# Optimization experiments

Measured on AMD Instinct MI355X. Metric: run time of the kernel, lower is better.

## Reference

```python
import jax, jax.numpy as jnp
import numpy as np

B, N, K = 128, 512, 6      # graphs, nodes per graph, kNN neighbors
IN_FEAT, POS_DIM, H = 128, 3, 256
NB = B * N                  # total nodes
EPS_BN = 1e-5


def setup_inputs() -> dict:
    key = jax.random.key(0)
    ks = jax.random.split(key, 32)
    inp = {
        "x": jax.random.normal(ks[0], (NB, IN_FEAT), dtype=jnp.float32),
        "pos": jax.random.normal(ks[1], (NB, POS_DIM), dtype=jnp.float32) * 5.0,
    }
    d_in = IN_FEAT + POS_DIM
    def lin(k, fi, fo):
        s = 1.0 / np.sqrt(fi)
        return jax.random.uniform(k, (fi, fo), jnp.float32, -s, s)
    # GCN layers
    inp["W1"] = lin(ks[2], d_in, H); inp["b1"] = jnp.zeros((H,), jnp.float32)
    inp["W2"] = lin(ks[3], H, H);    inp["b2"] = jnp.zeros((H,), jnp.float32)
    inp["W3"] = lin(ks[4], H, H);    inp["b3"] = jnp.zeros((H,), jnp.float32)
    # BatchNorm (eval mode: running stats)
    for i, km, kv in [(1, ks[5], ks[6]), (2, ks[7], ks[8]), (3, ks[9], ks[10])]:
        inp[f"g{i}"]  = jnp.ones((H,), jnp.float32)
        inp[f"be{i}"] = jnp.zeros((H,), jnp.float32)
        inp[f"m{i}"]  = jax.random.normal(km, (H,), jnp.float32) * 0.1
        inp[f"v{i}"]  = jax.random.uniform(kv, (H,), jnp.float32, 0.5, 1.5)
    # attention gate, heads
    inp["gate_w"] = lin(ks[11], H, 1); inp["gate_b"] = jnp.zeros((1,), jnp.float32)
    inp["aff_w"]  = lin(ks[12], H, 1); inp["aff_b"]  = jnp.zeros((1,), jnp.float32)
    inp["rl_w1"]  = lin(ks[13], H, H); inp["rl_b1"]  = jnp.zeros((H,), jnp.float32)
    inp["rl_w2"]  = lin(ks[14], H, POS_DIM); inp["rl_b2"] = jnp.zeros((POS_DIM,), jnp.float32)
    return inp


def _knn_edges(pos):
    # torch_geometric knn_graph semantics: per-graph k nearest neighbors,
    # no self loops, edges (neighbor -> node).  batch = repeat(arange(B), N).
    p = pos.reshape(B, N, POS_DIM)
    sq = jnp.sum(p * p, axis=-1)                                  # [B,N]
    d2 = sq[:, :, None] + sq[:, None, :] - 2.0 * jnp.einsum("bnd,bmd->bnm", p, p)
    d2 = jnp.where(jnp.eye(N, dtype=bool)[None], jnp.inf, d2)     # exclude self
    _, idx = jax.lax.top_k(-d2, K)                                # [B,N,K] local nbr ids
    offs = (jnp.arange(B) * N)[:, None, None]
    src = (idx + offs).reshape(-1)                                # neighbor (source)
    dst = jnp.repeat(jnp.arange(NB), K)                           # target node
    return src, dst


def _gcn(h, W, b, src, dst):
    # GCNConv: add self loops, symmetric norm D^-1/2 (A+I) D^-1/2
    hw = h @ W                                                    # [NB,H]
    deg = jax.ops.segment_sum(jnp.ones_like(dst, jnp.float32), dst, num_segments=NB) + 1.0
    dis = jax.lax.rsqrt(deg)
    norm = dis[src] * dis[dst]                                    # [E]
    agg = jax.ops.segment_sum(hw[src] * norm[:, None], dst, num_segments=NB)
    agg = agg + hw * (1.0 / deg)[:, None]                          # self loop term
    return agg + b


def _bn(h, g, be, m, v):
    return (h - m) * (g * jax.lax.rsqrt(v + EPS_BN)) + be


def reference(x, pos, W1, b1, W2, b2, W3, b3,
              g1, be1, m1, v1, g2, be2, m2, v2, g3, be3, m3, v3,
              gate_w, gate_b, aff_w, aff_b, rl_w1, rl_b1, rl_w2, rl_b2):
    src, dst = _knn_edges(pos)
    h = jnp.concatenate([x, pos], axis=1)                          # [NB, in_feat+3]
    h = jax.nn.relu(_bn(_gcn(h, W1, b1, src, dst), g1, be1, m1, v1))
    h = jax.nn.relu(_bn(_gcn(h, W2, b2, src, dst), g2, be2, m2, v2))
    h = jax.nn.relu(_bn(_gcn(h, W3, b3, src, dst), g3, be3, m3, v3))
    # (dropout is identity in eval mode)
    gate = jax.nn.relu(h @ gate_w + gate_b)[:, 0]                  # [NB]
    attn = jax.nn.softmax(gate.reshape(B, N), axis=1)              # scatter_softmax over batch
    gemb = jnp.einsum("bn,bnh->bh", attn, h.reshape(B, N, H))      # scatter_add of weighted x
    affinity = gemb @ aff_w + aff_b                                # [B,1]
    pose = jax.nn.relu(gemb @ rl_w1 + rl_b1) @ rl_w2 + rl_b2        # [B,3]
    return affinity, pose
```

## Files before the change

### kernel.cpp

```cpp
#include <hip/hip_runtime.h>
#include <hip/hip_bf16.h>
#include <math.h>
#include <float.h>

#define NBG 128
#define NND 512
#define KNN 6
#define NB_TOT (NBG*NND)
#define HF 256
#define NSTEP1 5

typedef short bf16x8 __attribute__((ext_vector_type(8)));
typedef float f32x4 __attribute__((ext_vector_type(4)));

__device__ __forceinline__ int swzoff(int row, int kbyte) {
    return (row*64 + kbyte) ^ (((row>>1)&3)<<4);
}

__device__ __forceinline__ void split_store(const float* v, char* hi_p, char* lo_p) {
    bf16x8 hi, lo;
    #pragma unroll
    for (int j = 0; j < 8; ++j) {
        __hip_bfloat16 h = __float2bfloat16(v[j]);
        float hf = __bfloat162float(h);
        __hip_bfloat16 l = __float2bfloat16(v[j] - hf);
        hi[j] = *(short*)&h;
        lo[j] = *(short*)&l;
    }
    *(bf16x8*)hi_p = hi;
    *(bf16x8*)lo_p = lo;
}

__device__ __forceinline__ int xcd_swz(int bid, int grid) {
    return (bid & 7) * (grid >> 3) + (bid >> 3);
}

__global__ __launch_bounds__(256) void knn_kernel(const float* __restrict__ pos,
                                                  unsigned short* __restrict__ nbr)
{
    const int blk = blockIdx.x;
    const int g = blk >> 3;
    const int chunk = (blk & 7) * 64;
    const int tid = threadIdx.x;
    const int node = chunk + (tid >> 2);
    const int sub = tid & 3;

    __shared__ float4 p4[NND + (NND>>6)];
    const float* pg = pos + (size_t)g * NND * 3;
    for (int n = tid; n < NND; n += 256) {
        float x = pg[n*3+0], y = pg[n*3+1], z = pg[n*3+2];
        p4[n + (n>>6)] = make_float4(x, y, z, x*x + y*y + z*z);
    }
    __syncthreads();

    const float4 pi = p4[node + (node>>6)];
    const float m2x = -2.0f*pi.x, m2y = -2.0f*pi.y, m2z = -2.0f*pi.z;

    float bdA[KNN], bdB[KNN]; int biA[KNN], biB[KNN];
    #pragma unroll
    for (int q = 0; q < KNN; ++q) {
        bdA[q] = FLT_MAX; biA[q] = 0x7fffffff;
        bdB[q] = FLT_MAX; biB[q] = 0x7fffffff;
    }

    const int j0 = sub * 128;
    const float4* baseA = &p4[sub*130];
    const float4* baseB = &p4[sub*130 + 65];

    #pragma unroll 2
    for (int t = 0; t < 64; ++t) {
        int ja = j0 + t, jb = j0 + 64 + t;
        float4 pa = baseA[t];
        float4 pb = baseB[t];
        float da = fmaf(m2z, pa.z, fmaf(m2y, pa.y, fmaf(m2x, pa.x, pa.w)));
        float db = fmaf(m2z, pb.z, fmaf(m2y, pb.y, fmaf(m2x, pb.x, pb.w)));
        da = (ja == node) ? FLT_MAX : da;
        db = (jb == node) ? FLT_MAX : db;
        float ca = da; int ia = ja;
        float cb = db; int ib = jb;
        #pragma unroll
        for (int q = 0; q < KNN; ++q) {
            bool sa = ca < bdA[q];
            float t1 = sa ? ca : bdA[q]; float t2 = sa ? bdA[q] : ca;
            int   t3 = sa ? ia : biA[q]; int   t4 = sa ? biA[q] : ia;
            bdA[q] = t1; ca = t2; biA[q] = t3; ia = t4;
            bool sb = cb < bdB[q];
            float u1 = sb ? cb : bdB[q]; float u2 = sb ? bdB[q] : cb;
            int   u3 = sb ? ib : biB[q]; int   u4 = sb ? biB[q] : ib;
            bdB[q] = u1; cb = u2; biB[q] = u3; ib = u4;
        }
    }

    float ld[KNN]; int li[KNN];
    #pragma unroll
    for (int q = 0; q < KNN; ++q) {
        float ad = bdA[q], xd = bdB[KNN-1-q];
        int   ai = biA[q], xi = biB[KNN-1-q];
        bool t = (ad < xd) || (ad == xd && ai < xi);
        ld[q] = t ? ad : xd;
        li[q] = t ? ai : xi;
    }
    #pragma unroll
    for (int pass = 0; pass < KNN-1; ++pass)
        #pragma unroll
        for (int a = 0; a < KNN-1-pass; ++a) {
            int b = a+1;
            bool sw = (ld[b] < ld[a]) || (ld[b] == ld[a] && li[b] < li[a]);
            float td = sw ? ld[b] : ld[a]; float ud = sw ? ld[a] : ld[b];
            int   ti = sw ? li[b] : li[a]; int   ui = sw ? li[a] : li[b];
            ld[a] = td; li[a] = ti; ld[b] = ud; li[b] = ui;
        }

    #pragma unroll
    for (int mi = 0; mi < 2; ++mi) {
        const int mask = 1 << mi;
        float od[KNN]; int oi[KNN];
        #pragma unroll
        for (int q = 0; q < KNN; ++q) {
            od[q] = __shfl_xor(ld[q], mask);
            oi[q] = __shfl_xor(li[q], mask);
        }
        #pragma unroll
        for (int q = 0; q < KNN; ++q) {
            float ad = ld[q], xd = od[KNN-1-q];
            int   ai = li[q], xi = oi[KNN-1-q];
            bool t = (ad < xd) || (ad == xd && ai < xi);
            ld[q] = t ? ad : xd;
            li[q] = t ? ai : xi;
        }
        #pragma unroll
        for (int pass = 0; pass < KNN-1; ++pass)
            #pragma unroll
            for (int a = 0; a < KNN-1-pass; ++a) {
                int b = a+1;
                bool sw = (ld[b] < ld[a]) || (ld[b] == ld[a] && li[b] < li[a]);
                float td = sw ? ld[b] : ld[a]; float ud = sw ? ld[a] : ld[b];
                int   ti = sw ? li[b] : li[a]; int   ui = sw ? li[a] : li[b];
                ld[a] = td; li[a] = ti; ld[b] = ud; li[b] = ui;
            }
    }

    if (sub == 0) {
        int base = (g*NND + node)*KNN;
        #pragma unroll
        for (int q = 0; q < KNN; ++q) nbr[base+q] = (unsigned short)li[q];
    }
}

__global__ __launch_bounds__(256) void prew_all(
    const float* __restrict__ W1, const float* __restrict__ W2,
    const float* __restrict__ W3,
    char* __restrict__ I1, char* __restrict__ I2, char* __restrict__ I3)
{
    int b = blockIdx.x;
    const float* W; char* img; int K, nstep;
    if (b < 20)      { W = W1; img = I1; K = 131; nstep = 5; }
    else if (b < 52) { W = W2; img = I2; K = 256; nstep = 8; b -= 20; }
    else             { W = W3; img = I3; K = 256; nstep = 8; b -= 52; }
    int gid = b*256 + threadIdx.x;
    int per_nb = nstep*512;
    int nb = gid / per_nb;
    int r  = gid - nb*per_nb;
    int step = r >> 9;
    int r2 = r & 511;
    int cl = r2 >> 2;
    int kc = (r2 & 3) * 8;
    float v[8];
    #pragma unroll
    for (int j = 0; j < 8; ++j) {
        int gk = step*32 + kc + j;
        v[j] = (gk < K) ? W[(size_t)gk*256 + nb*128 + cl] : 0.f;
    }
    char* base = img + (size_t)nb*nstep*16384 + (size_t)step*16384;
    int off = swzoff(cl, kc*2);
    split_store(v, base + off, base + 8192 + off);
}

__global__ __launch_bounds__(256) void agg_first(const float* __restrict__ x,
                                                 const float* __restrict__ pos,
                                                 const unsigned short* __restrict__ nbr,
                                                 char* __restrict__ Aimg)
{
    int gid = xcd_swz(blockIdx.x, gridDim.x)*256 + threadIdx.x;
    int i = gid / 20, ch = gid - i*20;
    const float rs = 1.0f/sqrtf(7.0f);
    const float c1 = rs*rs, c2 = 1.0f/7.0f;
    const int gbase = i & ~(NND-1);
    float v[8];
    if (ch < 16) {
        int jn[KNN];
        #pragma unroll
        for (int q = 0; q < KNN; ++q) jn[q] = gbase + nbr[i*KNN+q];
        const float4* x4 = (const float4*)x;
        int c4 = ch*2;
        float4 s0 = x4[(size_t)i*32 + c4], s1 = x4[(size_t)i*32 + c4 + 1];
        float a0=0,a1=0,a2=0,a3=0,b0=0,b1=0,b2=0,b3=0;
        #pragma unroll
        for (int q = 0; q < KNN; ++q) {
            float4 t0 = x4[(size_t)jn[q]*32 + c4];
            float4 t1 = x4[(size_t)jn[q]*32 + c4 + 1];
            a0+=t0.x; a1+=t0.y; a2+=t0.z; a3+=t0.w;
            b0+=t1.x; b1+=t1.y; b2+=t1.z; b3+=t1.w;
        }
        v[0]=a0*c1+s0.x*c2; v[1]=a1*c1+s0.y*c2; v[2]=a2*c1+s0.z*c2; v[3]=a3*c1+s0.w*c2;
        v[4]=b0*c1+s1.x*c2; v[5]=b1*c1+s1.y*c2; v[6]=b2*c1+s1.z*c2; v[7]=b3*c1+s1.w*c2;
    } else if (ch == 16) {
        int jn[KNN];
        #pragma unroll
        for (int q = 0; q < KNN; ++q) jn[q] = gbase + nbr[i*KNN+q];
        float ax=0, ay=0, az=0;
        #pragma unroll
        for (int q = 0; q < KNN; ++q) {
            ax += pos[(size_t)jn[q]*3+0];
            ay += pos[(size_t)jn[q]*3+1];
            az += pos[(size_t)jn[q]*3+2];
        }
        v[0] = ax*c1 + pos[(size_t)i*3+0]*c2;
        v[1] = ay*c1 + pos[(size_t)i*3+1]*c2;
        v[2] = az*c1 + pos[(size_t)i*3+2]*c2;
        v[3]=v[4]=v[5]=v[6]=v[7]=0.f;
    } else {
        #pragma unroll
        for (int j = 0; j < 8; ++j) v[j] = 0.f;
    }
    int mb = i >> 7, row = i & 127, step = ch >> 2, kbyte = (ch & 3)*16;
    char* base = Aimg + (size_t)mb*(NSTEP1*16384) + (size_t)step*16384;
    int off = swzoff(row, kbyte);
    split_store(v, base + off, base + 8192 + off);
}

__global__ __launch_bounds__(256) void agg_h(const float* __restrict__ h,
                                             const unsigned short* __restrict__ nbr,
                                             char* __restrict__ Aimg)
{
    int gid = xcd_swz(blockIdx.x, gridDim.x)*256 + threadIdx.x;
    int i = gid >> 5, ch = gid & 31;
    const float rs = 1.0f/sqrtf(7.0f);
    const float c1 = rs*rs, c2 = 1.0f/7.0f;
    const int gbase = i & ~(NND-1);
    int jn[KNN];
    #pragma unroll
    for (int q = 0; q < KNN; ++q) jn[q] = gbase + nbr[i*KNN+q];
    const float4* h4 = (const float4*)h;
    int c4 = ch*2;
    float4 s0 = h4[(size_t)i*64 + c4], s1 = h4[(size_t)i*64 + c4 + 1];
    float a0=0,a1=0,a2=0,a3=0,b0=0,b1=0,b2=0,b3=0;
    #pragma unroll
    for (int q = 0; q < KNN; ++q) {
        float4 t0 = h4[(size_t)jn[q]*64 + c4];
        float4 t1 = h4[(size_t)jn[q]*64 + c4 + 1];
        a0+=t0.x; a1+=t0.y; a2+=t0.z; a3+=t0.w;
        b0+=t1.x; b1+=t1.y; b2+=t1.z; b3+=t1.w;
    }
    float v[8];
    v[0]=a0*c1+s0.x*c2; v[1]=a1*c1+s0.y*c2; v[2]=a2*c1+s0.z*c2; v[3]=a3*c1+s0.w*c2;
    v[4]=b0*c1+s1.x*c2; v[5]=b1*c1+s1.y*c2; v[6]=b2*c1+s1.z*c2; v[7]=b3*c1+s1.w*c2;
    int mb = i >> 7, row = i & 127, step = ch >> 2, kbyte = (ch & 3)*16;
    char* base = Aimg + (size_t)mb*(8*16384) + (size_t)step*16384;
    int off = swzoff(row, kbyte);
    split_store(v, base + off, base + 8192 + off);
}

__global__ __launch_bounds__(256,4) void gemm_mfma(
    const char* __restrict__ Aimg, const char* __restrict__ Wimg, int nstep,
    const float* __restrict__ bias,
    const float* __restrict__ gam, const float* __restrict__ bet,
    const float* __restrict__ mu,  const float* __restrict__ var,
    float* __restrict__ out)
{
    __shared__ uint4 lds4[34816/16];
    char* lds  = (char*)lds4;
    char* Alds = lds;
    char* Wlds = lds + 16384;
    float* scs = (float*)(lds + 32768);
    float* shs = scs + 256;
    const int tid = threadIdx.x;
    const int lane = tid & 63, wave = tid >> 6;
    const int wm = wave >> 1, wn = wave & 1;
    const int mblk = blockIdx.x, nblk = blockIdx.y;

    if (tid < 256) {
        float s = gam[tid] / sqrtf(var[tid] + 1e-5f);
        scs[tid] = s;
        shs[tid] = bet[tid] + (bias[tid] - mu[tid]) * s;
    }

    const char* Ab = Aimg + (size_t)mblk * nstep * 16384;
    const char* Wb = Wimg + (size_t)nblk * nstep * 16384;

    const char* gbase; char* lbase;
    int soff;
    if (wave < 2) { gbase = Ab;  lbase = Alds; soff = wave*8192; }
    else          { gbase = Wb;  lbase = Wlds; soff = (wave-2)*8192; }

    f32x4 acc[4][4];
    #pragma unroll
    for (int m = 0; m < 4; ++m)
        #pragma unroll
        for (int n = 0; n < 4; ++n) acc[m][n] = (f32x4){0.f,0.f,0.f,0.f};

    for (int s = 0; s < nstep; ++s) {
        #pragma unroll
        for (int i = 0; i < 8; ++i) {
            int off = soff + i*1024;
            __builtin_amdgcn_global_load_lds(
                (const __attribute__((address_space(1))) void*)(gbase + (size_t)s*16384 + off + lane*16),
                (__attribute__((address_space(3))) void*)(lbase + off), 16, 0, 0);
        }
        __syncthreads();
        const int kb = (lane >> 4) * 16;
        bf16x8 ah[4], al[4];
        #pragma unroll
        for (int m = 0; m < 4; ++m) {
            int row = wm*64 + m*16 + (lane & 15);
            int off = swzoff(row, kb);
            ah[m] = *(const bf16x8*)(Alds + off);
            al[m] = *(const bf16x8*)(Alds + 8192 + off);
        }
        #pragma unroll
        for (int n = 0; n < 4; ++n) {
            int col = wn*64 + n*16 + (lane & 15);
            int off = swzoff(col, kb);
            bf16x8 bh = *(const bf16x8*)(Wlds + off);
            bf16x8 bl = *(const bf16x8*)(Wlds + 8192 + off);
            #pragma unroll
            for (int m = 0; m < 4; ++m) {
                acc[m][n] = __builtin_amdgcn_mfma_f32_16x16x32_bf16(ah[m], bh, acc[m][n], 0, 0, 0);
                acc[m][n] = __builtin_amdgcn_mfma_f32_16x16x32_bf16(al[m], bh, acc[m][n], 0, 0, 0);
                acc[m][n] = __builtin_amdgcn_mfma_f32_16x16x32_bf16(ah[m], bl, acc[m][n], 0, 0, 0);
            }
        }
        __syncthreads();
    }

    #pragma unroll
    for (int n = 0; n < 4; ++n) {
        int c = nblk*128 + wn*64 + n*16 + (lane & 15);
        float sc = scs[c], sh = shs[c];
        #pragma unroll
        for (int m = 0; m < 4; ++m) {
            int r0 = mblk*128 + wm*64 + m*16 + (lane >> 4)*4;
            #pragma unroll
            for (int q = 0; q < 4; ++q) {
                float v = acc[m][n][q]*sc + sh;
                out[(size_t)(r0+q)*256 + c] = fmaxf(v, 0.f);
            }
        }
    }
}

__global__ __launch_bounds__(256) void gate_kernel(const float* __restrict__ h3,
                                                   const float* __restrict__ gate_w,
                                                   const float* __restrict__ gate_b,
                                                   float* __restrict__ gate)
{
    const int lane = threadIdx.x & 63;
    const int gw = (blockIdx.x*256 + threadIdx.x) >> 6;
    float4 w4 = ((const float4*)gate_w)[lane];
    float gb = gate_b[0];
    #pragma unroll
    for (int it = 0; it < 4; ++it) {
        int r = gw + it*8192;
        float4 v = ((const float4*)(h3 + (size_t)r*HF))[lane];
        float s = v.x*w4.x + v.y*w4.y + v.z*w4.z + v.w*w4.w;
        #pragma unroll
        for (int o = 32; o > 0; o >>= 1) s += __shfl_xor(s, o, 64);
        if (lane == 0) gate[r] = fmaxf(s + gb, 0.f);
    }
}

__device__ __forceinline__ float blk_sum256(float v, volatile float* red)
{
    #pragma unroll
    for (int o = 32; o > 0; o >>= 1) v += __shfl_xor(v, o, 64);
    __syncthreads();
    if ((threadIdx.x & 63) == 0) red[threadIdx.x >> 6] = v;
    __syncthreads();
    return (red[0] + red[1]) + (red[2] + red[3]);
}

__global__ __launch_bounds__(256) void gemb_kernel(const float* __restrict__ h3,
                                                   const float* __restrict__ gate,
                                                   float* __restrict__ gembp)
{
    const int g = blockIdx.x, s = blockIdx.y;
    const int tid = threadIdx.x, lane = tid & 63, w = tid >> 6;
    __shared__ float at[128];
    __shared__ float red4[4][HF];
    __shared__ float red[4];

    float g0 = gate[g*NND + tid];
    float g1 = gate[g*NND + 256 + tid];
    float m = fmaxf(g0, g1);
    #pragma unroll
    for (int o = 32; o > 0; o >>= 1) m = fmaxf(m, __shfl_xor(m, o, 64));
    if ((tid & 63) == 0) red[tid >> 6] = m;
    __syncthreads();
    m = fmaxf(fmaxf(red[0], red[1]), fmaxf(red[2], red[3]));
    float S = blk_sum256(expf(g0 - m) + expf(g1 - m), red);
    if (tid < 128) at[tid] = expf(gate[g*NND + s*128 + tid] - m) / S;
    __syncthreads();

    const float* hb = h3 + (size_t)(g*NND + s*128 + w*32) * HF;
    float4 acc = make_float4(0.f, 0.f, 0.f, 0.f);
    #pragma unroll 4
    for (int n = 0; n < 32; ++n) {
        float a = at[w*32 + n];
        float4 v = ((const float4*)(hb + (size_t)n*HF))[lane];
        acc.x = fmaf(a, v.x, acc.x); acc.y = fmaf(a, v.y, acc.y);
        acc.z = fmaf(a, v.z, acc.z); acc.w = fmaf(a, v.w, acc.w);
    }
    *(float4*)&red4[w][lane*4] = acc;
    __syncthreads();
    if (tid < HF) {
        float sum = (red4[0][tid] + red4[1][tid]) + (red4[2][tid] + red4[3][tid]);
        gembp[((size_t)s*NBG + g)*HF + tid] = sum;
    }
}

__global__ __launch_bounds__(256) void heads_kernel(
    const float* __restrict__ gembp,
    const float* __restrict__ aff_w,  const float* __restrict__ aff_b,
    const float* __restrict__ rl_w1,  const float* __restrict__ rl_b1,
    const float* __restrict__ rl_w2,  const float* __restrict__ rl_b2,
    float* __restrict__ out)
{
    int g = blockIdx.x, tid = threadIdx.x;
    __shared__ float gemb[HF];
    __shared__ float red[4];
    float acc = (gembp[((size_t)0*NBG + g)*HF + tid] + gembp[((size_t)1*NBG + g)*HF + tid])
              + (gembp[((size_t)2*NBG + g)*HF + tid] + gembp[((size_t)3*NBG + g)*HF + tid]);
    gemb[tid] = acc;
    __syncthreads();

    float sa = blk_sum256(acc * aff_w[tid], red);
    if (tid == 0) out[g] = sa + aff_b[0];

    float t = rl_b1[tid];
    #pragma unroll 4
    for (int k2 = 0; k2 < HF; ++k2)
        t = fmaf(gemb[k2], rl_w1[(size_t)k2*HF + tid], t);
    t = fmaxf(t, 0.f);
    float s0 = blk_sum256(t * rl_w2[(size_t)tid*3 + 0], red);
    if (tid == 0) out[128 + g*3 + 0] = s0 + rl_b2[0];
    float s1 = blk_sum256(t * rl_w2[(size_t)tid*3 + 1], red);
    if (tid == 0) out[128 + g*3 + 1] = s1 + rl_b2[1];
    float s2 = blk_sum256(t * rl_w2[(size_t)tid*3 + 2], red);
    if (tid == 0) out[128 + g*3 + 2] = s2 + rl_b2[2];
}

extern "C" void kernel_launch(void* const* d_in, const int* in_sizes, int n_in,
                              void* d_out, int out_size, void* d_ws, size_t ws_size,
                              hipStream_t stream)
{
    const float* x      = (const float*)d_in[0];
    const float* pos    = (const float*)d_in[1];
    const float* W1     = (const float*)d_in[2];
    const float* b1     = (const float*)d_in[3];
    const float* W2     = (const float*)d_in[4];
    const float* b2     = (const float*)d_in[5];
    const float* W3     = (const float*)d_in[6];
    const float* b3     = (const float*)d_in[7];
    const float* g1     = (const float*)d_in[8];
    const float* be1    = (const float*)d_in[9];
    const float* m1     = (const float*)d_in[10];
    const float* v1     = (const float*)d_in[11];
    const float* g2     = (const float*)d_in[12];
    const float* be2    = (const float*)d_in[13];
    const float* m2     = (const float*)d_in[14];
    const float* v2     = (const float*)d_in[15];
    const float* g3     = (const float*)d_in[16];
    const float* be3    = (const float*)d_in[17];
    const float* m3     = (const float*)d_in[18];
    const float* v3     = (const float*)d_in[19];
    const float* gate_w = (const float*)d_in[20];
    const float* gate_b = (const float*)d_in[21];
    const float* aff_w  = (const float*)d_in[22];
    const float* aff_b  = (const float*)d_in[23];
    const float* rl_w1  = (const float*)d_in[24];
    const float* rl_b1  = (const float*)d_in[25];
    const float* rl_w2  = (const float*)d_in[26];
    const float* rl_b2  = (const float*)d_in[27];
    float* out = (float*)d_out;

    char* wsb = (char*)d_ws;
    unsigned short* nbr = (unsigned short*)wsb;
    char* Wimg1 = wsb + 786432;
    char* Wimg2 = Wimg1 + (size_t)2*NSTEP1*16384;
    char* Wimg3 = Wimg2 + (size_t)2*8*16384;
    float* h    = (float*)(Wimg3 + (size_t)2*8*16384);
    char* Aimg  = (char*)(h + (size_t)NB_TOT*HF);
    float* gate  = (float*)Aimg;
    float* gembp = gate + NB_TOT;

    knn_kernel<<<NBG*8, 256, 0, stream>>>(pos, nbr);
    prew_all<<<84, 256, 0, stream>>>(W1, W2, W3, Wimg1, Wimg2, Wimg3);

    agg_first<<<(NB_TOT*20)/256, 256, 0, stream>>>(x, pos, nbr, Aimg);
    gemm_mfma<<<dim3(NB_TOT/128, 2), 256, 0, stream>>>(Aimg, Wimg1, NSTEP1,
        b1, g1, be1, m1, v1, h);
    agg_h<<<(NB_TOT*32)/256, 256, 0, stream>>>(h, nbr, Aimg);
    gemm_mfma<<<dim3(NB_TOT/128, 2), 256, 0, stream>>>(Aimg, Wimg2, 8,
        b2, g2, be2, m2, v2, h);
    agg_h<<<(NB_TOT*32)/256, 256, 0, stream>>>(h, nbr, Aimg);
    gemm_mfma<<<dim3(NB_TOT/128, 2), 256, 0, stream>>>(Aimg, Wimg3, 8,
        b3, g3, be3, m3, v3, h);

    gate_kernel<<<2048, 256, 0, stream>>>(h, gate_w, gate_b, gate);
    gemb_kernel<<<dim3(NBG, 4), 256, 0, stream>>>(h, gate, gembp);
    heads_kernel<<<NBG, 256, 0, stream>>>(gembp, aff_w, aff_b,
                                          rl_w1, rl_b1, rl_w2, rl_b2, out);
}
```

Measured before the change: 241.6 us.

## Fuse neighbor aggregation into GEMM for GCN layers 2 and 3

Replaces the separate agg_h kernel and the gemm_mfma launch for layers 2 and 3 with one gcn_fused kernel. Each 512-thread block gathers the neighbor-averaged features for its 128 rows straight into LDS as split bf16, then multiplies against the full 256-column weight. This removes the round trip of the split-bf16 A image through global memory and two kernel launches per layer. In exchange, the gather latency is no longer overlapped across separate kernels, occupancy drops to 2 blocks per CU, and ping-pong h buffers are needed.

```diff
diff --git a/kernel.cpp b/kernel.cpp
--- a/kernel.cpp
+++ b/kernel.cpp
@@ -229,38 +229,6 @@
     split_store(v, base + off, base + 8192 + off);
 }
 
-__global__ __launch_bounds__(256) void agg_h(const float* __restrict__ h,
-                                             const unsigned short* __restrict__ nbr,
-                                             char* __restrict__ Aimg)
-{
-    int gid = xcd_swz(blockIdx.x, gridDim.x)*256 + threadIdx.x;
-    int i = gid >> 5, ch = gid & 31;
-    const float rs = 1.0f/sqrtf(7.0f);
-    const float c1 = rs*rs, c2 = 1.0f/7.0f;
-    const int gbase = i & ~(NND-1);
-    int jn[KNN];
-    #pragma unroll
-    for (int q = 0; q < KNN; ++q) jn[q] = gbase + nbr[i*KNN+q];
-    const float4* h4 = (const float4*)h;
-    int c4 = ch*2;
-    float4 s0 = h4[(size_t)i*64 + c4], s1 = h4[(size_t)i*64 + c4 + 1];
-    float a0=0,a1=0,a2=0,a3=0,b0=0,b1=0,b2=0,b3=0;
-    #pragma unroll
-    for (int q = 0; q < KNN; ++q) {
-        float4 t0 = h4[(size_t)jn[q]*64 + c4];
-        float4 t1 = h4[(size_t)jn[q]*64 + c4 + 1];
-        a0+=t0.x; a1+=t0.y; a2+=t0.z; a3+=t0.w;
-        b0+=t1.x; b1+=t1.y; b2+=t1.z; b3+=t1.w;
-    }
-    float v[8];
-    v[0]=a0*c1+s0.x*c2; v[1]=a1*c1+s0.y*c2; v[2]=a2*c1+s0.z*c2; v[3]=a3*c1+s0.w*c2;
-    v[4]=b0*c1+s1.x*c2; v[5]=b1*c1+s1.y*c2; v[6]=b2*c1+s1.z*c2; v[7]=b3*c1+s1.w*c2;
-    int mb = i >> 7, row = i & 127, step = ch >> 2, kbyte = (ch & 3)*16;
-    char* base = Aimg + (size_t)mb*(8*16384) + (size_t)step*16384;
-    int off = swzoff(row, kbyte);
-    split_store(v, base + off, base + 8192 + off);
-}
-
 __global__ __launch_bounds__(256,4) void gemm_mfma(
     const char* __restrict__ Aimg, const char* __restrict__ Wimg, int nstep,
     const float* __restrict__ bias,
@@ -344,6 +312,118 @@
             for (int q = 0; q < 4; ++q) {
                 float v = acc[m][n][q]*sc + sh;
                 out[(size_t)(r0+q)*256 + c] = fmaxf(v, 0.f);
+            }
+        }
+    }
+}
+
+__global__ __launch_bounds__(512,2) void gcn_fused(
+    const float* __restrict__ hin,
+    const unsigned short* __restrict__ nbr,
+    const char* __restrict__ Wimg,
+    const float* __restrict__ bias,
+    const float* __restrict__ gam, const float* __restrict__ bet,
+    const float* __restrict__ mu,  const float* __restrict__ var,
+    float* __restrict__ hout)
+{
+    __shared__ uint4 lds4[51200/16];
+    char* Alds = (char*)lds4;
+    char* Wlds = (char*)lds4 + 16384;
+    float* scs = (float*)((char*)lds4 + 49152);
+    float* shs = scs + 256;
+    const int tid = threadIdx.x;
+    const int lane = tid & 63, wave = tid >> 6;
+    const int wm = wave >> 2, wn = wave & 3;
+    const int mblk = xcd_swz(blockIdx.x, gridDim.x);
+
+    if (tid < 256) {
+        float s = gam[tid] / sqrtf(var[tid] + 1e-5f);
+        scs[tid] = s;
+        shs[tid] = bet[tid] + (bias[tid] - mu[tid]) * s;
+    }
+
+    const int arow = tid >> 2, ch = tid & 3;
+    const int gnode = mblk*128 + arow;
+    const int gb = gnode & ~(NND-1);
+    int jn[KNN];
+    #pragma unroll
+    for (int q = 0; q < KNN; ++q) jn[q] = gb + nbr[gnode*KNN + q];
+    const float rs = 1.0f/sqrtf(7.0f);
+    const float c1 = rs*rs, c2 = 1.0f/7.0f;
+    const int aoff = swzoff(arow, ch*16);
+    const float4* h4 = (const float4*)hin;
+
+    f32x4 acc[4][4];
+    #pragma unroll
+    for (int m = 0; m < 4; ++m)
+        #pragma unroll
+        for (int n = 0; n < 4; ++n) acc[m][n] = (f32x4){0.f,0.f,0.f,0.f};
+
+    for (int s = 0; s < 8; ++s) {
+        #pragma unroll
+        for (int i = 0; i < 4; ++i) {
+            int woff = i*8192 + wave*1024;
+            size_t srcoff = (i < 2) ? ((size_t)s*16384 + woff)
+                                    : ((size_t)(8+s)*16384 + (woff - 16384));
+            __builtin_amdgcn_global_load_lds(
+                (const __attribute__((address_space(1))) void*)(Wimg + srcoff + lane*16),
+                (__attribute__((address_space(3))) void*)(Wlds + woff), 16, 0, 0);
+        }
+        {
+            const int fb = s*8 + ch*2;
+            float a0=0,a1=0,a2=0,a3=0,b0=0,b1=0,b2=0,b3=0;
+            #pragma unroll
+            for (int q = 0; q < KNN; ++q) {
+                float4 t0 = h4[(size_t)jn[q]*64 + fb];
+                float4 t1 = h4[(size_t)jn[q]*64 + fb + 1];
+                a0+=t0.x; a1+=t0.y; a2+=t0.z; a3+=t0.w;
+                b0+=t1.x; b1+=t1.y; b2+=t1.z; b3+=t1.w;
+            }
+            float4 s0 = h4[(size_t)gnode*64 + fb];
+            float4 s1 = h4[(size_t)gnode*64 + fb + 1];
+            float v[8];
+            v[0]=a0*c1+s0.x*c2; v[1]=a1*c1+s0.y*c2; v[2]=a2*c1+s0.z*c2; v[3]=a3*c1+s0.w*c2;
+            v[4]=b0*c1+s1.x*c2; v[5]=b1*c1+s1.y*c2; v[6]=b2*c1+s1.z*c2; v[7]=b3*c1+s1.w*c2;
+            split_store(v, Alds + aoff, Alds + 8192 + aoff);
+        }
+        __syncthreads();
+        const int kb = (lane >> 4) * 16;
+        bf16x8 ah[4], al[4];
+        #pragma unroll
+        for (int m = 0; m < 4; ++m) {
+            int r = wm*64 + m*16 + (lane & 15);
+            int o = swzoff(r, kb);
+            ah[m] = *(const bf16x8*)(Alds + o);
+            al[m] = *(const bf16x8*)(Alds + 8192 + o);
+        }
+        const char* wreg = Wlds + ((wn >= 2) ? 16384 : 0);
+        #pragma unroll
+        for (int n = 0; n < 4; ++n) {
+            int cl = (wn & 1)*64 + n*16 + (lane & 15);
+            int o = swzoff(cl, kb);
+            bf16x8 bh = *(const bf16x8*)(wreg + o);
+            bf16x8 bl = *(const bf16x8*)(wreg + 8192 + o);
+            #pragma unroll
+            for (int m = 0; m < 4; ++m) {
+                acc[m][n] = __builtin_amdgcn_mfma_f32_16x16x32_bf16(ah[m], bh, acc[m][n], 0, 0, 0);
+                acc[m][n] = __builtin_amdgcn_mfma_f32_16x16x32_bf16(al[m], bh, acc[m][n], 0, 0, 0);
+                acc[m][n] = __builtin_amdgcn_mfma_f32_16x16x32_bf16(ah[m], bl, acc[m][n], 0, 0, 0);
+            }
+        }
+        __syncthreads();
+    }
+
+    #pragma unroll
+    for (int n = 0; n < 4; ++n) {
+        int c = wn*64 + n*16 + (lane & 15);
+        float sc = scs[c], sh = shs[c];
+        #pragma unroll
+        for (int m = 0; m < 4; ++m) {
+            int r0 = mblk*128 + wm*64 + m*16 + (lane >> 4)*4;
+            #pragma unroll
+            for (int q = 0; q < 4; ++q) {
+                float v = acc[m][n][q]*sc + sh;
+                hout[(size_t)(r0+q)*256 + c] = fmaxf(v, 0.f);
             }
         }
     }
@@ -488,26 +568,26 @@
     char* Wimg1 = wsb + 786432;
     char* Wimg2 = Wimg1 + (size_t)2*NSTEP1*16384;
     char* Wimg3 = Wimg2 + (size_t)2*8*16384;
-    float* h    = (float*)(Wimg3 + (size_t)2*8*16384);
-    char* Aimg  = (char*)(h + (size_t)NB_TOT*HF);
-    float* gate  = (float*)Aimg;
-    float* gembp = gate + NB_TOT;
+    float* h_a  = (float*)(Wimg3 + (size_t)2*8*16384);
+    char* regB  = (char*)(h_a + (size_t)NB_TOT*HF);
+    char*  Aimg  = regB;
+    float* h_b   = (float*)regB;
+    float* gate  = (float*)regB;
+    float* gembp = (float*)(regB + (size_t)NB_TOT*4);
 
     knn_kernel<<<NBG*8, 256, 0, stream>>>(pos, nbr);
     prew_all<<<84, 256, 0, stream>>>(W1, W2, W3, Wimg1, Wimg2, Wimg3);
 
     agg_first<<<(NB_TOT*20)/256, 256, 0, stream>>>(x, pos, nbr, Aimg);
     gemm_mfma<<<dim3(NB_TOT/128, 2), 256, 0, stream>>>(Aimg, Wimg1, NSTEP1,
-        b1, g1, be1, m1, v1, h);
-    agg_h<<<(NB_TOT*32)/256, 256, 0, stream>>>(h, nbr, Aimg);
-    gemm_mfma<<<dim3(NB_TOT/128, 2), 256, 0, stream>>>(Aimg, Wimg2, 8,
-        b2, g2, be2, m2, v2, h);
-    agg_h<<<(NB_TOT*32)/256, 256, 0, stream>>>(h, nbr, Aimg);
-    gemm_mfma<<<dim3(NB_TOT/128, 2), 256, 0, stream>>>(Aimg, Wimg3, 8,
-        b3, g3, be3, m3, v3, h);
-
-    gate_kernel<<<2048, 256, 0, stream>>>(h, gate_w, gate_b, gate);
-    gemb_kernel<<<dim3(NBG, 4), 256, 0, stream>>>(h, gate, gembp);
+        b1, g1, be1, m1, v1, h_a);
+    gcn_fused<<<NB_TOT/128, 512, 0, stream>>>(h_a, nbr, Wimg2,
+        b2, g2, be2, m2, v2, h_b);
+    gcn_fused<<<NB_TOT/128, 512, 0, stream>>>(h_b, nbr, Wimg3,
+        b3, g3, be3, m3, v3, h_a);
+
+    gate_kernel<<<2048, 256, 0, stream>>>(h_a, gate_w, gate_b, gate);
+    gemb_kernel<<<dim3(NBG, 4), 256, 0, stream>>>(h_a, gate, gembp);
     heads_kernel<<<NBG, 256, 0, stream>>>(gembp, aff_w, aff_b,
                                           rl_w1, rl_b1, rl_w2, rl_b2, out);
 }
```

Result: faster. 229.8 us (-4.9%).
